# Kernel optimization log

Measured on AMD Instinct MI355X. Metric: run time of the kernel, lower is better.

## Reference

```python
import jax, jax.numpy as jnp
import numpy as np

N_GRAPHS = 128
N_NODES = 512
N = N_GRAPHS * N_NODES      # 65536 total nodes
E = 524288                  # edges (avg degree 8)
F_IN = 4                    # num_features
EMB = 4                     # embedding_dim
HEADS = 4
GDIM = 16                   # GATConv_dim
D = GDIM * HEADS            # 64 = d_model
NHEAD = 2                   # heads // 2
FF = 64                     # ff_hid_dim
OUT = 64                    # output_dim
N_GAT_REST = 3              # gat_layers - 1


def setup_inputs() -> dict:
    key = jax.random.key(0)
    ks = iter(jax.random.split(key, 64))
    def nrm(shape, fan_in):
        return jax.random.normal(next(ks), shape, jnp.float32) / np.float32(np.sqrt(fan_in))
    inp = {}
    inp['x'] = jax.random.normal(next(ks), (N, F_IN), jnp.float32)
    inp['edge_index'] = jax.random.randint(next(ks), (2, E), 0, N, dtype=jnp.int32)
    inp['batch'] = jnp.repeat(jnp.arange(N_GRAPHS, dtype=jnp.int32), N_NODES)
    # feature_fc
    inp['Wf'] = nrm((F_IN, EMB), F_IN); inp['bf'] = jnp.zeros((EMB,), jnp.float32)
    # input GATConv (EMB -> HEADS*GDIM)
    inp['gW0'] = nrm((EMB, HEADS * GDIM), EMB)
    inp['aS0'] = nrm((HEADS, GDIM), GDIM); inp['aD0'] = nrm((HEADS, GDIM), GDIM)
    inp['gb0'] = jnp.zeros((D,), jnp.float32)
    # remaining 3 GATConv layers (D -> HEADS*GDIM), stacked
    inp['gW'] = nrm((N_GAT_REST, D, HEADS * GDIM), D)
    inp['aS'] = nrm((N_GAT_REST, HEADS, GDIM), GDIM); inp['aD'] = nrm((N_GAT_REST, HEADS, GDIM), GDIM)
    inp['gb'] = jnp.zeros((N_GAT_REST, D), jnp.float32)
    # decoder layer: self-attn, cross-attn, layernorms, FFN
    for p in ['sWq','sWk','sWv','sWo','cWq','cWk','cWv','cWo']:
        inp[p] = nrm((D, D), D)
    for p in ['sbq','sbk','sbv','sbo','cbq','cbk','cbv','cbo']:
        inp[p] = jnp.zeros((D,), jnp.float32)
    for g, b in [('ln1g','ln1b'), ('ln2g','ln2b'), ('ln3g','ln3b')]:
        inp[g] = jnp.ones((D,), jnp.float32); inp[b] = jnp.zeros((D,), jnp.float32)
    inp['ffW1'] = nrm((D, FF), D); inp['ffb1'] = jnp.zeros((FF,), jnp.float32)
    inp['ffW2'] = nrm((FF, D), FF); inp['ffb2'] = jnp.zeros((D,), jnp.float32)
    inp['fcW'] = nrm((D, OUT), D); inp['fcb'] = jnp.zeros((OUT,), jnp.float32)
    return inp


def _gat(h_in, src, dst, W, a_s, a_d, b):
    # PyG GATConv, concat=True, negative_slope=0.2, self-loops already in (src,dst)
    h = (h_in @ W).reshape(N, HEADS, GDIM)
    es = jnp.einsum('nho,ho->nh', h, a_s)   # [N,H]
    ed = jnp.einsum('nho,ho->nh', h, a_d)
    e = jax.nn.leaky_relu(es[src] + ed[dst], 0.2)          # [E',H]
    m = jax.ops.segment_max(e, dst, num_segments=N)        # segment softmax over dst
    w = jnp.exp(e - m[dst])
    s = jax.ops.segment_sum(w, dst, num_segments=N)
    alpha = w / (s[dst] + 1e-16)
    out = jax.ops.segment_sum(h[src] * alpha[..., None], dst, num_segments=N)
    return out.reshape(N, D) + b


def _mha(q, kv, Wq, bq, Wk, bk, Wv, bv, Wo, bo):
    B, S, Dm = q.shape
    hd = Dm // NHEAD
    Q = (q @ Wq + bq).reshape(B, S, NHEAD, hd)
    K = (kv @ Wk + bk).reshape(B, S, NHEAD, hd)
    V = (kv @ Wv + bv).reshape(B, S, NHEAD, hd)
    a = jax.nn.softmax(jnp.einsum('bqhd,bkhd->bhqk', Q, K) / jnp.sqrt(jnp.float32(hd)), axis=-1)
    o = jnp.einsum('bhqk,bkhd->bqhd', a, V).reshape(B, S, Dm)
    return o @ Wo + bo


def _ln(x, g, b):
    m = x.mean(-1, keepdims=True)
    v = ((x - m) ** 2).mean(-1, keepdims=True)
    return (x - m) / jnp.sqrt(v + 1e-5) * g + b


def reference(x, edge_index, batch, Wf, bf, gW0, aS0, aD0, gb0, gW, aS, aD, gb,
              sWq, sWk, sWv, sWo, cWq, cWk, cWv, cWo,
              sbq, sbk, sbv, sbo, cbq, cbk, cbv, cbo,
              ln1g, ln1b, ln2g, ln2b, ln3g, ln3b,
              ffW1, ffb1, ffW2, ffb2, fcW, fcb):
    loops = jnp.arange(N, dtype=edge_index.dtype)
    src = jnp.concatenate([edge_index[0], loops])
    dst = jnp.concatenate([edge_index[1], loops])
    h = x @ Wf + bf
    h = jax.nn.leaky_relu(_gat(h, src, dst, gW0, aS0, aD0, gb0), 0.01)
    for i in range(N_GAT_REST):
        h = jax.nn.leaky_relu(_gat(h, src, dst, gW[i], aS[i], aD[i], gb[i]), 0.01)
    t = h.reshape(N_GRAPHS, N_NODES, D)
    # one transformer decoder layer, post-norm, memory = layer input
    mem = t
    t = _ln(t + _mha(t, t, sWq, sbq, sWk, sbk, sWv, sbv, sWo, sbo), ln1g, ln1b)
    t = _ln(t + _mha(t, mem, cWq, cbq, cWk, cbk, cWv, cbv, cWo, cbo), ln2g, ln2b)
    t = _ln(t + (jax.nn.relu(t @ ffW1 + ffb1) @ ffW2 + ffb2), ln3g, ln3b)
    h = t.reshape(N, D)
    pooled = jax.ops.segment_sum(h, batch, num_segments=N_GRAPHS) / jnp.float32(N_NODES)
    return pooled @ fcW + fcb
```

## Files before the change

### kernel.cpp

```cpp
#include <hip/hip_runtime.h>
#include <math.h>

#define NG 128
#define SEQ 512
#define NN 65536
#define EE 524288
#define DM 64

typedef __attribute__((ext_vector_type(8))) short short8;
typedef __attribute__((ext_vector_type(4))) float f32x4;

__device__ __forceinline__ float lrelu(float x, float s){ return x > 0.f ? x : s*x; }

__device__ __forceinline__ unsigned short f2bf(float x){
  union { float f; unsigned u; } v; v.f = x;
  unsigned r = v.u + 0x7FFF + ((v.u>>16)&1);
  return (unsigned short)(r>>16);
}
__device__ __forceinline__ float bf2f(unsigned short x){
  union { unsigned u; float f; } v; v.u = ((unsigned)x)<<16;
  return v.f;
}

__global__ void k_count(const int* __restrict__ dst, int* __restrict__ deg){
  int e = blockIdx.x*256 + threadIdx.x;
  atomicAdd(&deg[dst[e]], 1);
}

__global__ void k_scan1(const int* __restrict__ deg, int* __restrict__ excl, int* __restrict__ bsums){
  __shared__ int sm[256];
  int tid = threadIdx.x;
  int i = blockIdx.x*256 + tid;
  int v = deg[i];
  sm[tid] = v;
  __syncthreads();
  int val = v;
  for (int off=1; off<256; off<<=1){
    int add = (tid>=off)? sm[tid-off] : 0;
    __syncthreads();
    val += add;
    sm[tid] = val;
    __syncthreads();
  }
  excl[i] = val - v;
  if (tid==255) bsums[blockIdx.x] = val;
}

__global__ void k_scan2(int* __restrict__ bsums){
  __shared__ int sm[256];
  int tid=threadIdx.x;
  int v = bsums[tid];
  sm[tid]=v;
  __syncthreads();
  int val=v;
  for (int off=1; off<256; off<<=1){
    int add = (tid>=off)? sm[tid-off]:0;
    __syncthreads();
    val += add;
    sm[tid]=val;
    __syncthreads();
  }
  bsums[tid] = val - v;
}

__global__ void k_scan3(const int* __restrict__ excl, const int* __restrict__ bsums,
                        int* __restrict__ rowp, int* __restrict__ cursor){
  int i = blockIdx.x*256 + threadIdx.x;
  int v = excl[i] + bsums[blockIdx.x];
  rowp[i]=v; cursor[i]=v;
  if (i==0) rowp[NN]=EE;
}

__global__ void k_fill(const int* __restrict__ src, const int* __restrict__ dst,
                       int* __restrict__ cursor, int* __restrict__ col){
  int e = blockIdx.x*256 + threadIdx.x;
  int d = dst[e];
  int p = atomicAdd(&cursor[d], 1);
  col[p] = src[e];
}

__global__ void k_w0(const float* __restrict__ Wf, const float* __restrict__ bf,
                     const float* __restrict__ gW0, float* __restrict__ W0c, float* __restrict__ b0c){
  int j = threadIdx.x;
  float b = 0.f;
  for (int k=0;k<4;k++) b += bf[k]*gW0[k*64+j];
  b0c[j]=b;
  for (int i=0;i<4;i++){
    float s=0.f;
    for(int k=0;k<4;k++) s += Wf[i*4+k]*gW0[k*64+j];
    W0c[i*64+j]=s;
  }
}

template<int DIN, int BIAS>
__global__ void __launch_bounds__(256) k_transform(const float* __restrict__ hin, const float* __restrict__ W,
                            const float* __restrict__ bias,
                            const float* __restrict__ aSp, const float* __restrict__ aDp,
                            unsigned short* __restrict__ hout, float* __restrict__ es, float* __restrict__ ed){
  __shared__ float inL[DIN][68];
  __shared__ float Wl[DIN][64];
  __shared__ float asl[64], adl[64];
  int tid = threadIdx.x;
  int n0 = blockIdx.x*64;
  if (tid < 64){ asl[tid] = aSp[tid]; adl[tid] = aDp[tid]; }
  for (int idx=tid; idx<DIN*16; idx+=256){
    int k = idx>>4, jj = (idx&15)<<2;
    *(float4*)&Wl[k][jj] = *(const float4*)&W[k*64+jj];
  }
  for (int idx=tid; idx<64*(DIN/4); idx+=256){
    int node = idx/(DIN/4), kk = (idx%(DIN/4))*4;
    float4 v = *(const float4*)&hin[(size_t)(n0+node)*DIN + kk];
    inL[kk][node]=v.x; inL[kk+1][node]=v.y; inL[kk+2][node]=v.z; inL[kk+3][node]=v.w;
  }
  __syncthreads();
  int i = tid>>4, j = tid&15;
  float acc[4][4];
  #pragma unroll
  for (int r=0;r<4;r++){
    #pragma unroll
    for (int c=0;c<4;c++) acc[r][c] = 0.f;
  }
  #pragma unroll 4
  for (int k=0;k<DIN;k++){
    float4 av = *(float4*)&inL[k][4*i];
    float4 bv = *(float4*)&Wl[k][4*j];
    float a_[4]={av.x,av.y,av.z,av.w}, b_[4]={bv.x,bv.y,bv.z,bv.w};
    #pragma unroll
    for (int r=0;r<4;r++){
      #pragma unroll
      for (int c=0;c<4;c++) acc[r][c] += a_[r]*b_[c];
    }
  }
  float4 asv = *(float4*)&asl[4*j];
  float4 adv = *(float4*)&adl[4*j];
  float bb[4] = {0.f,0.f,0.f,0.f};
  if (BIAS){
    float4 bv = *(const float4*)&bias[4*j];
    bb[0]=bv.x; bb[1]=bv.y; bb[2]=bv.z; bb[3]=bv.w;
  }
  #pragma unroll
  for (int r=0;r<4;r++){
    float y0=acc[r][0]+bb[0], y1=acc[r][1]+bb[1], y2=acc[r][2]+bb[2], y3=acc[r][3]+bb[3];
    int node = n0 + 4*i + r;
    ushort4 hv;
    hv.x=f2bf(y0); hv.y=f2bf(y1); hv.z=f2bf(y2); hv.w=f2bf(y3);
    *(ushort4*)&hout[(size_t)node*64 + 4*j] = hv;
    float ps = y0*asv.x + y1*asv.y + y2*asv.z + y3*asv.w;
    float pd = y0*adv.x + y1*adv.y + y2*adv.z + y3*adv.w;
    ps += __shfl_xor(ps,1); ps += __shfl_xor(ps,2);
    pd += __shfl_xor(pd,1); pd += __shfl_xor(pd,2);
    if ((j&3)==0){
      es[(size_t)node*4 + (j>>2)] = ps;
      ed[(size_t)node*4 + (j>>2)] = pd;
    }
  }
}

__global__ void __launch_bounds__(256) k_transform_bf(const unsigned short* __restrict__ hin, const float* __restrict__ W,
                            const float* __restrict__ aSp, const float* __restrict__ aDp,
                            unsigned short* __restrict__ hout, float* __restrict__ es, float* __restrict__ ed){
  __shared__ float inL[64][68];
  __shared__ float Wl[64][64];
  __shared__ float asl[64], adl[64];
  int tid = threadIdx.x;
  int n0 = blockIdx.x*64;
  if (tid < 64){ asl[tid] = aSp[tid]; adl[tid] = aDp[tid]; }
  for (int idx=tid; idx<1024; idx+=256){
    int k = idx>>4, jj = (idx&15)<<2;
    *(float4*)&Wl[k][jj] = *(const float4*)&W[k*64+jj];
  }
  for (int idx=tid; idx<1024; idx+=256){
    int node = idx>>4, kk = (idx&15)<<2;
    ushort4 v = *(const ushort4*)&hin[(size_t)(n0+node)*64 + kk];
    inL[kk][node]=bf2f(v.x); inL[kk+1][node]=bf2f(v.y); inL[kk+2][node]=bf2f(v.z); inL[kk+3][node]=bf2f(v.w);
  }
  __syncthreads();
  int i = tid>>4, j = tid&15;
  float acc[4][4];
  #pragma unroll
  for (int r=0;r<4;r++){
    #pragma unroll
    for (int c=0;c<4;c++) acc[r][c] = 0.f;
  }
  #pragma unroll 4
  for (int k=0;k<64;k++){
    float4 av = *(float4*)&inL[k][4*i];
    float4 bv = *(float4*)&Wl[k][4*j];
    float a_[4]={av.x,av.y,av.z,av.w}, b_[4]={bv.x,bv.y,bv.z,bv.w};
    #pragma unroll
    for (int r=0;r<4;r++){
      #pragma unroll
      for (int c=0;c<4;c++) acc[r][c] += a_[r]*b_[c];
    }
  }
  float4 asv = *(float4*)&asl[4*j];
  float4 adv = *(float4*)&adl[4*j];
  #pragma unroll
  for (int r=0;r<4;r++){
    float y0=acc[r][0], y1=acc[r][1], y2=acc[r][2], y3=acc[r][3];
    int node = n0 + 4*i + r;
    ushort4 hv;
    hv.x=f2bf(y0); hv.y=f2bf(y1); hv.z=f2bf(y2); hv.w=f2bf(y3);
    *(ushort4*)&hout[(size_t)node*64 + 4*j] = hv;
    float ps = y0*asv.x + y1*asv.y + y2*asv.z + y3*asv.w;
    float pd = y0*adv.x + y1*adv.y + y2*adv.z + y3*adv.w;
    ps += __shfl_xor(ps,1); ps += __shfl_xor(ps,2);
    pd += __shfl_xor(pd,1); pd += __shfl_xor(pd,2);
    if ((j&3)==0){
      es[(size_t)node*4 + (j>>2)] = ps;
      ed[(size_t)node*4 + (j>>2)] = pd;
    }
  }
}

template<int BF16OUT>
__global__ void __launch_bounds__(256) k_aggregate(const unsigned short* __restrict__ h, const float* __restrict__ es,
                            const float* __restrict__ ed, const int* __restrict__ rowp,
                            const int* __restrict__ col, const float* __restrict__ gb,
                            void* __restrict__ houtv){
  int tid = threadIdx.x;
  int n = blockIdx.x*4 + (tid>>6);
  int l = tid&63;
  int q = l>>4;
  int sl = l&15;
  int head = sl>>2;
  float edn = ed[(size_t)n*4 + head];
  float es_self = es[(size_t)n*4 + head];
  int beg = __builtin_amdgcn_readfirstlane(rowp[n]);
  int end = __builtin_amdgcn_readfirstlane(rowp[n+1]);
  float m = -1e30f, s = 0.f;
  float a0=0.f, a1=0.f, a2=0.f, a3=0.f;
  int i = beg;
  for (; i+8 <= end; i += 8){
    int c0=col[i], c1=col[i+1], c2=col[i+2], c3=col[i+3];
    int c4=col[i+4], c5=col[i+5], c6=col[i+6], c7=col[i+7];
    int t01 = (q&1)? c1 : c0;
    int t23 = (q&1)? c3 : c2;
    int sq0 = (q&2)? t23 : t01;
    int t45 = (q&1)? c5 : c4;
    int t67 = (q&1)? c7 : c6;
    int sq1 = (q&2)? t67 : t45;
    ushort4 hv0 = *(const ushort4*)&h[(size_t)sq0*64 + 4*sl];
    ushort4 hv1 = *(const ushort4*)&h[(size_t)sq1*64 + 4*sl];
    float e0 = lrelu(es[(size_t)sq0*4+head] + edn, 0.2f);
    float e1 = lrelu(es[(size_t)sq1*4+head] + edn, 0.2f);
    float mx = fmaxf(e0, e1);
    if (__any(mx > m + 8.f)){
      float nm = fmaxf(m, mx);
      float c = __expf(m - nm);
      s*=c; a0*=c; a1*=c; a2*=c; a3*=c; m = nm;
    }
    float w0 = __expf(e0 - m);
    float w1 = __expf(e1 - m);
    s += w0 + w1;
    a0 += w0*bf2f(hv0.x) + w1*bf2f(hv1.x);
    a1 += w0*bf2f(hv0.y) + w1*bf2f(hv1.y);
    a2 += w0*bf2f(hv0.z) + w1*bf2f(hv1.z);
    a3 += w0*bf2f(hv0.w) + w1*bf2f(hv1.w);
  }
  if (i < end){
    int last = end-1;
    int i1=(i+1<last)?i+1:last, i2=(i+2<last)?i+2:last, i3=(i+3<last)?i+3:last;
    int i4=(i+4<last)?i+4:last, i5=(i+5<last)?i+5:last, i6=(i+6<last)?i+6:last;
    int c0=col[i], c1=col[i1], c2=col[i2], c3=col[i3];
    int c4=col[i4], c5=col[i5], c6=col[i6], c7=col[last];
    int t01 = (q&1)? c1 : c0;
    int t23 = (q&1)? c3 : c2;
    int sq0 = (q&2)? t23 : t01;
    int t45 = (q&1)? c5 : c4;
    int t67 = (q&1)? c7 : c6;
    int sq1 = (q&2)? t67 : t45;
    bool ac0 = (i + q) < end;
    bool ac1 = (i + 4 + q) < end;
    ushort4 hv0 = *(const ushort4*)&h[(size_t)sq0*64 + 4*sl];
    ushort4 hv1 = *(const ushort4*)&h[(size_t)sq1*64 + 4*sl];
    float e0 = lrelu(es[(size_t)sq0*4+head] + edn, 0.2f);
    float e1 = lrelu(es[(size_t)sq1*4+head] + edn, 0.2f);
    if (!ac0) e0 = -1e30f;
    if (!ac1) e1 = -1e30f;
    float mx = fmaxf(e0, e1);
    if (__any(mx > m + 8.f)){
      float nm = fmaxf(m, mx);
      float c = __expf(m - nm);
      s*=c; a0*=c; a1*=c; a2*=c; a3*=c; m = nm;
    }
    float w0 = ac0 ? __expf(e0 - m) : 0.f;
    float w1 = ac1 ? __expf(e1 - m) : 0.f;
    s += w0 + w1;
    a0 += w0*bf2f(hv0.x) + w1*bf2f(hv1.x);
    a1 += w0*bf2f(hv0.y) + w1*bf2f(hv1.y);
    a2 += w0*bf2f(hv0.z) + w1*bf2f(hv1.z);
    a3 += w0*bf2f(hv0.w) + w1*bf2f(hv1.w);
  }
  #pragma unroll
  for (int off=16; off<=32; off<<=1){
    float m2 = __shfl_xor(m, off);
    float s2 = __shfl_xor(s, off);
    float b0 = __shfl_xor(a0, off);
    float b1 = __shfl_xor(a1, off);
    float b2 = __shfl_xor(a2, off);
    float b3 = __shfl_xor(a3, off);
    float nm = fmaxf(m, m2);
    float c1 = __expf(m - nm), c2 = __expf(m2 - nm);
    s  = s*c1  + s2*c2;
    a0 = a0*c1 + b0*c2;
    a1 = a1*c1 + b1*c2;
    a2 = a2*c1 + b2*c2;
    a3 = a3*c1 + b3*c2;
    m = nm;
  }
  {
    float e_self = lrelu(es_self + edn, 0.2f);
    float nm = fmaxf(m, e_self);
    float c = __expf(m - nm), cs = __expf(e_self - nm);
    ushort4 hs = *(const ushort4*)&h[(size_t)n*64 + 4*sl];
    s  = s*c  + cs;
    a0 = a0*c + cs*bf2f(hs.x);
    a1 = a1*c + cs*bf2f(hs.y);
    a2 = a2*c + cs*bf2f(hs.z);
    a3 = a3*c + cs*bf2f(hs.w);
  }
  if (q == 0){
    float inv = 1.f/(s + 1e-16f);
    float4 gv = *(const float4*)&gb[4*sl];
    float o0 = lrelu(a0*inv + gv.x, 0.01f);
    float o1 = lrelu(a1*inv + gv.y, 0.01f);
    float o2 = lrelu(a2*inv + gv.z, 0.01f);
    float o3 = lrelu(a3*inv + gv.w, 0.01f);
    if (BF16OUT){
      ushort4 hv; hv.x=f2bf(o0); hv.y=f2bf(o1); hv.z=f2bf(o2); hv.w=f2bf(o3);
      *(ushort4*)((unsigned short*)houtv + (size_t)n*64 + 4*sl) = hv;
    } else {
      *(float4*)((float*)houtv + (size_t)n*64 + 4*sl) = make_float4(o0,o1,o2,o3);
    }
  }
}

__global__ void __launch_bounds__(256) k_qkv3(const float* __restrict__ in0, const float* __restrict__ W0, const float* __restrict__ b0, unsigned short* __restrict__ o0,
                      const float* __restrict__ in1, const float* __restrict__ W1, const float* __restrict__ b1, unsigned short* __restrict__ o1,
                      const float* __restrict__ in2, const float* __restrict__ W2, const float* __restrict__ b2, unsigned short* __restrict__ o2,
                      float scl0){
  __shared__ float inL[64][68];
  __shared__ float Wl[64][64];
  int tid = threadIdx.x;
  int n0 = blockIdx.x*64;
  int i = tid>>4, j = tid&15;
  const float* ins[3] = {in0, in1, in2};
  const float* Ws[3] = {W0, W1, W2};
  const float* bs[3] = {b0, b1, b2};
  unsigned short* os[3] = {o0, o1, o2};
  const float* cur = nullptr;
  for (int w=0; w<3; w++){
    __syncthreads();
    if (ins[w] != cur){
      cur = ins[w];
      for (int idx=tid; idx<1024; idx+=256){
        int node = idx>>4, kk = (idx&15)<<2;
        float4 v = *(const float4*)&cur[(size_t)(n0+node)*64 + kk];
        inL[kk][node]=v.x; inL[kk+1][node]=v.y; inL[kk+2][node]=v.z; inL[kk+3][node]=v.w;
      }
    }
    for (int idx=tid; idx<1024; idx+=256){
      int k = idx>>4, jj = (idx&15)<<2;
      *(float4*)&Wl[k][jj] = *(const float4*)&Ws[w][k*64+jj];
    }
    __syncthreads();
    float acc[4][4];
    #pragma unroll
    for (int r=0;r<4;r++){
      #pragma unroll
      for (int c=0;c<4;c++) acc[r][c] = 0.f;
    }
    #pragma unroll 4
    for (int k=0;k<64;k++){
      float4 av = *(float4*)&inL[k][4*i];
      float4 bv = *(float4*)&Wl[k][4*j];
      float a_[4]={av.x,av.y,av.z,av.w}, b_[4]={bv.x,bv.y,bv.z,bv.w};
      #pragma unroll
      for (int r=0;r<4;r++){
        #pragma unroll
        for (int c=0;c<4;c++) acc[r][c] += a_[r]*b_[c];
      }
    }
    float4 bv = *(const float4*)&bs[w][4*j];
    float bb[4] = {bv.x, bv.y, bv.z, bv.w};
    float sc = (w==0) ? scl0 : 1.f;
    #pragma unroll
    for (int r=0;r<4;r++){
      ushort4 hv;
      hv.x = f2bf((acc[r][0]+bb[0])*sc);
      hv.y = f2bf((acc[r][1]+bb[1])*sc);
      hv.z = f2bf((acc[r][2]+bb[2])*sc);
      hv.w = f2bf((acc[r][3]+bb[3])*sc);
      *(ushort4*)&os[w][(size_t)(n0+4*i+r)*64 + 4*j] = hv;
    }
  }
}

__global__ void __launch_bounds__(256) k_resln_bf(const unsigned short* __restrict__ in, const float* __restrict__ W,
                               const float* __restrict__ b, const float* __restrict__ res,
                               const float* __restrict__ g, const float* __restrict__ bl,
                               float* __restrict__ out){
  __shared__ float inL[64][68];
  __shared__ float Wl[64][64];
  int tid = threadIdx.x;
  int n0 = blockIdx.x*64;
  for (int idx=tid; idx<1024; idx+=256){
    int k = idx>>4, jj = (idx&15)<<2;
    *(float4*)&Wl[k][jj] = *(const float4*)&W[k*64+jj];
  }
  for (int idx=tid; idx<1024; idx+=256){
    int node = idx>>4, kk = (idx&15)<<2;
    ushort4 v = *(const ushort4*)&in[(size_t)(n0+node)*64 + kk];
    inL[kk][node]=bf2f(v.x); inL[kk+1][node]=bf2f(v.y); inL[kk+2][node]=bf2f(v.z); inL[kk+3][node]=bf2f(v.w);
  }
  __syncthreads();
  int i = tid>>4, j = tid&15;
  float acc[4][4];
  #pragma unroll
  for (int r=0;r<4;r++){
    #pragma unroll
    for (int c=0;c<4;c++) acc[r][c] = 0.f;
  }
  #pragma unroll 4
  for (int k=0;k<64;k++){
    float4 av = *(float4*)&inL[k][4*i];
    float4 bv = *(float4*)&Wl[k][4*j];
    float a_[4]={av.x,av.y,av.z,av.w}, b_[4]={bv.x,bv.y,bv.z,bv.w};
    #pragma unroll
    for (int r=0;r<4;r++){
      #pragma unroll
      for (int c=0;c<4;c++) acc[r][c] += a_[r]*b_[c];
    }
  }
  float4 bv = *(const float4*)&b[4*j];
  float bb[4] = {bv.x, bv.y, bv.z, bv.w};
  float4 gv = *(const float4*)&g[4*j];
  float4 blv = *(const float4*)&bl[4*j];
  float gg[4] = {gv.x, gv.y, gv.z, gv.w};
  float bb2[4] = {blv.x, blv.y, blv.z, blv.w};
  #pragma unroll
  for (int r=0;r<4;r++){
    int node = n0 + 4*i + r;
    float4 rv = *(const float4*)&res[(size_t)node*64 + 4*j];
    float y[4] = {acc[r][0]+bb[0]+rv.x, acc[r][1]+bb[1]+rv.y,
                  acc[r][2]+bb[2]+rv.z, acc[r][3]+bb[3]+rv.w};
    float s = (y[0]+y[1]) + (y[2]+y[3]);
    s += __shfl_xor(s,1); s += __shfl_xor(s,2); s += __shfl_xor(s,4); s += __shfl_xor(s,8);
    float mean = s * (1.f/64.f);
    float d[4] = {y[0]-mean, y[1]-mean, y[2]-mean, y[3]-mean};
    float v = (d[0]*d[0]+d[1]*d[1]) + (d[2]*d[2]+d[3]*d[3]);
    v += __shfl_xor(v,1); v += __shfl_xor(v,2); v += __shfl_xor(v,4); v += __shfl_xor(v,8);
    float inv = rsqrtf(v*(1.f/64.f) + 1e-5f);
    *(float4*)&out[(size_t)node*64 + 4*j] =
      make_float4(d[0]*inv*gg[0]+bb2[0], d[1]*inv*gg[1]+bb2[1],
                  d[2]*inv*gg[2]+bb2[2], d[3]*inv*gg[3]+bb2[3]);
  }
}

__global__ void __launch_bounds__(256) k_ffn(const float* __restrict__ in,
                     const float* __restrict__ W1p, const float* __restrict__ b1p,
                     const float* __restrict__ W2p, const float* __restrict__ b2p,
                     const float* __restrict__ g, const float* __restrict__ bl,
                     float* __restrict__ out){
  __shared__ float inL[64][68];
  __shared__ float Wl[64][64];
  __shared__ float ffL[64][68];
  int tid = threadIdx.x;
  int n0 = blockIdx.x*64;
  for (int idx=tid; idx<1024; idx+=256){
    int k = idx>>4, jj = (idx&15)<<2;
    *(float4*)&Wl[k][jj] = *(const float4*)&W1p[k*64+jj];
  }
  for (int idx=tid; idx<1024; idx+=256){
    int node = idx>>4, kk = (idx&15)<<2;
    float4 v = *(const float4*)&in[(size_t)(n0+node)*64 + kk];
    inL[kk][node]=v.x; inL[kk+1][node]=v.y; inL[kk+2][node]=v.z; inL[kk+3][node]=v.w;
  }
  __syncthreads();
  int i = tid>>4, j = tid&15;
  float acc[4][4];
  #pragma unroll
  for (int r=0;r<4;r++){
    #pragma unroll
    for (int c=0;c<4;c++) acc[r][c] = 0.f;
  }
  #pragma unroll 4
  for (int k=0;k<64;k++){
    float4 av = *(float4*)&inL[k][4*i];
    float4 bv = *(float4*)&Wl[k][4*j];
    float a_[4]={av.x,av.y,av.z,av.w}, b_[4]={bv.x,bv.y,bv.z,bv.w};
    #pragma unroll
    for (int r=0;r<4;r++){
      #pragma unroll
      for (int c=0;c<4;c++) acc[r][c] += a_[r]*b_[c];
    }
  }
  float4 b1v = *(const float4*)&b1p[4*j];
  float bb1[4] = {b1v.x, b1v.y, b1v.z, b1v.w};
  #pragma unroll
  for (int r=0;r<4;r++){
    #pragma unroll
    for (int c=0;c<4;c++){
      ffL[4*j+c][4*i+r] = fmaxf(acc[r][c] + bb1[c], 0.f);
    }
  }
  __syncthreads();
  for (int idx=tid; idx<1024; idx+=256){
    int k = idx>>4, jj = (idx&15)<<2;
    *(float4*)&Wl[k][jj] = *(const float4*)&W2p[k*64+jj];
  }
  __syncthreads();
  #pragma unroll
  for (int r=0;r<4;r++){
    #pragma unroll
    for (int c=0;c<4;c++) acc[r][c] = 0.f;
  }
  #pragma unroll 4
  for (int k=0;k<64;k++){
    float4 av = *(float4*)&ffL[k][4*i];
    float4 bv = *(float4*)&Wl[k][4*j];
    float a_[4]={av.x,av.y,av.z,av.w}, b_[4]={bv.x,bv.y,bv.z,bv.w};
    #pragma unroll
    for (int r=0;r<4;r++){
      #pragma unroll
      for (int c=0;c<4;c++) acc[r][c] += a_[r]*b_[c];
    }
  }
  float4 b2v = *(const float4*)&b2p[4*j];
  float bb2v[4] = {b2v.x, b2v.y, b2v.z, b2v.w};
  float4 gv = *(const float4*)&g[4*j];
  float4 blv = *(const float4*)&bl[4*j];
  float gg[4] = {gv.x, gv.y, gv.z, gv.w};
  float bbl[4] = {blv.x, blv.y, blv.z, blv.w};
  #pragma unroll
  for (int r=0;r<4;r++){
    int node = n0 + 4*i + r;
    float y[4];
    #pragma unroll
    for (int c=0;c<4;c++) y[c] = acc[r][c] + bb2v[c] + inL[4*j+c][4*i+r];
    float s = (y[0]+y[1]) + (y[2]+y[3]);
    s += __shfl_xor(s,1); s += __shfl_xor(s,2); s += __shfl_xor(s,4); s += __shfl_xor(s,8);
    float mean = s * (1.f/64.f);
    float d[4] = {y[0]-mean, y[1]-mean, y[2]-mean, y[3]-mean};
    float v = (d[0]*d[0]+d[1]*d[1]) + (d[2]*d[2]+d[3]*d[3]);
    v += __shfl_xor(v,1); v += __shfl_xor(v,2); v += __shfl_xor(v,4); v += __shfl_xor(v,8);
    float inv = rsqrtf(v*(1.f/64.f) + 1e-5f);
    *(float4*)&out[(size_t)node*64 + 4*j] =
      make_float4(d[0]*inv*gg[0]+bbl[0], d[1]*inv*gg[1]+bbl[1],
                  d[2]*inv*gg[2]+bbl[2], d[3]*inv*gg[3]+bbl[3]);
  }
}

__global__ void __launch_bounds__(512, 4) k_attn(const unsigned short* __restrict__ Q, const unsigned short* __restrict__ K,
                      const unsigned short* __restrict__ V, unsigned short* __restrict__ Out){
  __shared__ char smem[40960];
  char* Ksm = smem;
  char* Vsm = smem + 16384;
  char* Psm = smem + 32768;

  int bid = blockIdx.x;
  int qh = bid & 1;
  int h  = (bid>>1) & 1;
  int b  = bid>>2;
  int tid = threadIdx.x;
  int wave = tid>>6;
  int l = tid & 63;
  int lq = l & 15;
  int g  = l >> 4;
  const size_t hb = (size_t)b*SEQ*64 + (size_t)h*32;
  const f32x4 zero = {0.f,0.f,0.f,0.f};

  int qbase = qh*256 + wave*32;
  short8 qf[2];
  f32x4 O[2][2];
  float m_[2], l_[2];
  #pragma unroll
  for (int qt=0; qt<2; qt++){
    qf[qt] = *(const short8*)(Q + hb + (size_t)(qbase + qt*16 + lq)*64 + g*8);
    O[qt][0] = zero; O[qt][1] = zero;
    m_[qt] = -1e30f; l_[qt] = 0.f;
  }

  char* Pw = Psm + wave*1024;

  for (int ph=0; ph<2; ph++){
    __syncthreads();
    #pragma unroll
    for (int it=0; it<2; it++){
      int i = tid + it*512;
      int row = i>>2, j = i&3;
      uint4 v = *(const uint4*)(K + hb + (size_t)(ph*256 + row)*64 + j*8);
      *(uint4*)(Ksm + row*64 + ((j*16) ^ (((row>>1)&3)<<4))) = v;
    }
    #pragma unroll
    for (int it=0; it<2; it++){
      int i = tid + it*512;
      int key = i>>2, j = i&3;
      uint4 vv = *(const uint4*)(V + hb + (size_t)(ph*256 + key)*64 + j*8);
      const unsigned short* vs = (const unsigned short*)&vv;
      #pragma unroll
      for (int c=0;c<8;c++){
        int d = j*8 + c;
        *(unsigned short*)(Vsm + d*512 + ((key*2) ^ ((d&7)<<4))) = vs[c];
      }
    }
    __syncthreads();
    for (int p=0; p<8; p++){
      int r0 = p*32 + lq, r1 = r0 + 16;
      short8 kf0 = *(short8*)(Ksm + r0*64 + ((g*16) ^ (((r0>>1)&3)<<4)));
      short8 kf1 = *(short8*)(Ksm + r1*64 + ((g*16) ^ (((r1>>1)&3)<<4)));
      int d0 = lq, d1 = lq + 16;
      short8 vt0 = *(short8*)(Vsm + d0*512 + ((p*64 + g*16) ^ ((d0&7)<<4)));
      short8 vt1 = *(short8*)(Vsm + d1*512 + ((p*64 + g*16) ^ ((d1&7)<<4)));
      int swzp = ((lq>>1)&3)<<4;
      #pragma unroll
      for (int qt=0; qt<2; qt++){
        f32x4 s0 = __builtin_amdgcn_mfma_f32_16x16x32_bf16(kf0, qf[qt], zero, 0,0,0);
        f32x4 s1 = __builtin_amdgcn_mfma_f32_16x16x32_bf16(kf1, qf[qt], zero, 0,0,0);
        float pmax = fmaxf(fmaxf(fmaxf(s0.x,s0.y),fmaxf(s0.z,s0.w)),
                           fmaxf(fmaxf(s1.x,s1.y),fmaxf(s1.z,s1.w)));
        pmax = fmaxf(pmax, __shfl_xor(pmax, 16));
        pmax = fmaxf(pmax, __shfl_xor(pmax, 32));
        float mn = fmaxf(m_[qt], pmax);
        float corr = __expf(m_[qt] - mn);
        m_[qt] = mn;
        float e0 = __expf(s0.x - mn), e1 = __expf(s0.y - mn);
        float e2 = __expf(s0.z - mn), e3 = __expf(s0.w - mn);
        float e4 = __expf(s1.x - mn), e5 = __expf(s1.y - mn);
        float e6 = __expf(s1.z - mn), e7 = __expf(s1.w - mn);
        l_[qt] = l_[qt]*corr + (((e0+e1)+(e2+e3)) + ((e4+e5)+(e6+e7)));
        O[qt][0] *= corr; O[qt][1] *= corr;
        uint2 w0, w1;
        w0.x = (unsigned)f2bf(e0) | ((unsigned)f2bf(e1)<<16);
        w0.y = (unsigned)f2bf(e2) | ((unsigned)f2bf(e3)<<16);
        w1.x = (unsigned)f2bf(e4) | ((unsigned)f2bf(e5)<<16);
        w1.y = (unsigned)f2bf(e6) | ((unsigned)f2bf(e7)<<16);
        *(uint2*)(Pw + lq*64 + ((g*8) ^ swzp)) = w0;
        *(uint2*)(Pw + lq*64 + ((32 + g*8) ^ swzp)) = w1;
        short8 pb = *(short8*)(Pw + lq*64 + ((g*16) ^ swzp));
        O[qt][0] = __builtin_amdgcn_mfma_f32_16x16x32_bf16(vt0, pb, O[qt][0], 0,0,0);
        O[qt][1] = __builtin_amdgcn_mfma_f32_16x16x32_bf16(vt1, pb, O[qt][1], 0,0,0);
      }
    }
  }
  #pragma unroll
  for (int qt=0; qt<2; qt++){
    float lt = l_[qt];
    lt += __shfl_xor(lt, 16);
    lt += __shfl_xor(lt, 32);
    float inv = 1.f/lt;
    unsigned short* op = Out + hb + (size_t)(qbase + qt*16 + lq)*64;
    ushort4 o0, o1;
    o0.x=f2bf(O[qt][0].x*inv); o0.y=f2bf(O[qt][0].y*inv); o0.z=f2bf(O[qt][0].z*inv); o0.w=f2bf(O[qt][0].w*inv);
    o1.x=f2bf(O[qt][1].x*inv); o1.y=f2bf(O[qt][1].y*inv); o1.z=f2bf(O[qt][1].z*inv); o1.w=f2bf(O[qt][1].w*inv);
    *(ushort4*)(op + g*4) = o0;
    *(ushort4*)(op + 16 + g*4) = o1;
  }
}

__global__ void __launch_bounds__(256) k_pool_fc(const float* __restrict__ t, const float* __restrict__ fcW,
                          const float* __restrict__ fcb, float* __restrict__ out){
  __shared__ float pl[4][64];
  __shared__ float pf[64];
  int b = blockIdx.x;
  int tid = threadIdx.x;
  int j = tid&63, seg = tid>>6;
  const float* basep = t + (size_t)b*SEQ*64;
  float s = 0.f;
  for (int si=seg*128; si<(seg+1)*128; si++) s += basep[(size_t)si*64 + j];
  pl[seg][j] = s;
  __syncthreads();
  if (tid < 64){
    pf[tid] = (pl[0][tid]+pl[1][tid]+pl[2][tid]+pl[3][tid]) * (1.f/512.f);
  }
  __syncthreads();
  if (tid < 64){
    float o = fcb[tid];
    for (int k=0;k<64;k++) o += pf[k]*fcW[k*64+tid];
    out[(size_t)b*64 + tid] = o;
  }
}

extern "C" void kernel_launch(void* const* d_in, const int* in_sizes, int n_in,
                              void* d_out, int out_size, void* d_ws, size_t ws_size,
                              hipStream_t stream) {
  const float* x    = (const float*)d_in[0];
  const int*   ei   = (const int*)d_in[1];
  const float* Wf   = (const float*)d_in[3];
  const float* bf   = (const float*)d_in[4];
  const float* gW0  = (const float*)d_in[5];
  const float* aS0  = (const float*)d_in[6];
  const float* aD0  = (const float*)d_in[7];
  const float* gb0  = (const float*)d_in[8];
  const float* gW   = (const float*)d_in[9];
  const float* aS   = (const float*)d_in[10];
  const float* aD   = (const float*)d_in[11];
  const float* gb   = (const float*)d_in[12];
  const float* sWq  = (const float*)d_in[13];
  const float* sWk  = (const float*)d_in[14];
  const float* sWv  = (const float*)d_in[15];
  const float* sWo  = (const float*)d_in[16];
  const float* cWq  = (const float*)d_in[17];
  const float* cWk  = (const float*)d_in[18];
  const float* cWv  = (const float*)d_in[19];
  const float* cWo  = (const float*)d_in[20];
  const float* sbq  = (const float*)d_in[21];
  const float* sbk  = (const float*)d_in[22];
  const float* sbv  = (const float*)d_in[23];
  const float* sbo  = (const float*)d_in[24];
  const float* cbq  = (const float*)d_in[25];
  const float* cbk  = (const float*)d_in[26];
  const float* cbv  = (const float*)d_in[27];
  const float* cbo  = (const float*)d_in[28];
  const float* ln1g = (const float*)d_in[29];
  const float* ln1b = (const float*)d_in[30];
  const float* ln2g = (const float*)d_in[31];
  const float* ln2b = (const float*)d_in[32];
  const float* ln3g = (const float*)d_in[33];
  const float* ln3b = (const float*)d_in[34];
  const float* ffW1 = (const float*)d_in[35];
  const float* ffb1 = (const float*)d_in[36];
  const float* ffW2 = (const float*)d_in[37];
  const float* ffb2 = (const float*)d_in[38];
  const float* fcW  = (const float*)d_in[39];
  const float* fcb  = (const float*)d_in[40];

  char* ws = (char*)d_ws;
  size_t off = 0;
  auto alloc = [&](size_t bytes) -> void* {
    void* p = ws + off;
    off += (bytes + 255) & ~(size_t)255;
    return p;
  };
  int* deg    = (int*)alloc(NN*sizeof(int));
  int* excl   = (int*)alloc(NN*sizeof(int));
  int* rowp   = (int*)alloc((NN+1)*sizeof(int));
  int* cursor = (int*)alloc(NN*sizeof(int));
  int* col    = (int*)alloc(EE*sizeof(int));
  int* bsums  = (int*)alloc(256*sizeof(int));
  float* W0c  = (float*)alloc(4*64*sizeof(float));
  float* b0c  = (float*)alloc(64*sizeof(float));
  float* es   = (float*)alloc((size_t)NN*4*sizeof(float));
  float* ed   = (float*)alloc((size_t)NN*4*sizeof(float));
  unsigned short* Hb   = (unsigned short*)alloc((size_t)NN*64*sizeof(unsigned short));
  unsigned short* Hagg = (unsigned short*)alloc((size_t)NN*64*sizeof(unsigned short));
  unsigned short* Qb = (unsigned short*)alloc((size_t)NN*64*sizeof(unsigned short));
  unsigned short* Kb = (unsigned short*)alloc((size_t)NN*64*sizeof(unsigned short));
  unsigned short* Vb = (unsigned short*)alloc((size_t)NN*64*sizeof(unsigned short));
  unsigned short* Ob = (unsigned short*)alloc((size_t)NN*64*sizeof(unsigned short));
  float* B1   = (float*)alloc((size_t)NN*64*sizeof(float));
  float* B2   = (float*)alloc((size_t)NN*64*sizeof(float));
  float* B5   = (float*)alloc((size_t)NN*64*sizeof(float));

  const int* e_src = ei;
  const int* e_dst = ei + EE;

  const float scale = 0.17677669529663687f;

  hipMemsetAsync(deg, 0, NN*sizeof(int), stream);
  k_count<<<EE/256, 256, 0, stream>>>(e_dst, deg);
  k_scan1<<<NN/256, 256, 0, stream>>>(deg, excl, bsums);
  k_scan2<<<1, 256, 0, stream>>>(bsums);
  k_scan3<<<NN/256, 256, 0, stream>>>(excl, bsums, rowp, cursor);
  k_fill<<<EE/256, 256, 0, stream>>>(e_src, e_dst, cursor, col);

  k_w0<<<1, 64, 0, stream>>>(Wf, bf, gW0, W0c, b0c);

  k_transform<4,1><<<NN/64, 256, 0, stream>>>(x, W0c, b0c, aS0, aD0, Hb, es, ed);
  k_aggregate<1><<<NN/4, 256, 0, stream>>>(Hb, es, ed, rowp, col, gb0, Hagg);
  k_transform_bf<<<NN/64, 256, 0, stream>>>(Hagg, gW+0*4096, aS+0*64, aD+0*64, Hb, es, ed);
  k_aggregate<1><<<NN/4, 256, 0, stream>>>(Hb, es, ed, rowp, col, gb+0*64, Hagg);
  k_transform_bf<<<NN/64, 256, 0, stream>>>(Hagg, gW+1*4096, aS+1*64, aD+1*64, Hb, es, ed);
  k_aggregate<1><<<NN/4, 256, 0, stream>>>(Hb, es, ed, rowp, col, gb+1*64, Hagg);
  k_transform_bf<<<NN/64, 256, 0, stream>>>(Hagg, gW+2*4096, aS+2*64, aD+2*64, Hb, es, ed);
  k_aggregate<0><<<NN/4, 256, 0, stream>>>(Hb, es, ed, rowp, col, gb+2*64, B2);

  k_qkv3<<<NN/64, 256, 0, stream>>>(B2, sWq, sbq, Qb, B2, sWk, sbk, Kb, B2, sWv, sbv, Vb, scale);
  k_attn<<<NG*2*2, 512, 0, stream>>>(Qb, Kb, Vb, Ob);
  k_resln_bf<<<NN/64, 256, 0, stream>>>(Ob, sWo, sbo, B2, ln1g, ln1b, B5);

  k_qkv3<<<NN/64, 256, 0, stream>>>(B5, cWq, cbq, Qb, B2, cWk, cbk, Kb, B2, cWv, cbv, Vb, scale);
  k_attn<<<NG*2*2, 512, 0, stream>>>(Qb, Kb, Vb, Ob);
  k_resln_bf<<<NN/64, 256, 0, stream>>>(Ob, cWo, cbo, B5, ln2g, ln2b, B2);

  k_ffn<<<NN/64, 256, 0, stream>>>(B2, ffW1, ffb1, ffW2, ffb2, ln3g, ln3b, B1);

  k_pool_fc<<<NG, 256, 0, stream>>>(B1, fcW, fcb, (float*)d_out);
}
```

Baseline: 409.4 us.

## Interleave source attention scores into padded feature rows and fuse weight premultiply

The per-node source attention scores (es) are now stored inside each bf16 feature row, which is padded to a stride of 80 elements, instead of in a separate array. The aggregation gather can then fetch the neighbor's features and its score from the same row rather than making a second random access into another array. The tiny k_w0 launch is also folded into the first transform kernel, which recomputes the combined weight and bias per block. The cost is a 25% larger H buffer (160-byte rows) and some redundant per-block weight math.

```diff
diff --git a/kernel.cpp b/kernel.cpp
--- a/kernel.cpp
+++ b/kernel.cpp
@@ -6,6 +6,7 @@
 #define NN 65536
 #define EE 524288
 #define DM 64
+#define HSTR 80
 
 typedef __attribute__((ext_vector_type(8))) short short8;
 typedef __attribute__((ext_vector_type(4))) float f32x4;
@@ -79,38 +80,34 @@
   col[p] = src[e];
 }
 
-__global__ void k_w0(const float* __restrict__ Wf, const float* __restrict__ bf,
-                     const float* __restrict__ gW0, float* __restrict__ W0c, float* __restrict__ b0c){
-  int j = threadIdx.x;
-  float b = 0.f;
-  for (int k=0;k<4;k++) b += bf[k]*gW0[k*64+j];
-  b0c[j]=b;
-  for (int i=0;i<4;i++){
-    float s=0.f;
-    for(int k=0;k<4;k++) s += Wf[i*4+k]*gW0[k*64+j];
-    W0c[i*64+j]=s;
-  }
-}
-
-template<int DIN, int BIAS>
-__global__ void __launch_bounds__(256) k_transform(const float* __restrict__ hin, const float* __restrict__ W,
-                            const float* __restrict__ bias,
+__global__ void __launch_bounds__(256) k_transform0(const float* __restrict__ x,
+                            const float* __restrict__ Wf, const float* __restrict__ bf,
+                            const float* __restrict__ gW0,
                             const float* __restrict__ aSp, const float* __restrict__ aDp,
-                            unsigned short* __restrict__ hout, float* __restrict__ es, float* __restrict__ ed){
-  __shared__ float inL[DIN][68];
-  __shared__ float Wl[DIN][64];
+                            unsigned short* __restrict__ hout, float* __restrict__ ed){
+  __shared__ float inL[4][68];
+  __shared__ float Wl[4][64];
+  __shared__ float b0l[64];
   __shared__ float asl[64], adl[64];
   int tid = threadIdx.x;
   int n0 = blockIdx.x*64;
-  if (tid < 64){ asl[tid] = aSp[tid]; adl[tid] = aDp[tid]; }
-  for (int idx=tid; idx<DIN*16; idx+=256){
-    int k = idx>>4, jj = (idx&15)<<2;
-    *(float4*)&Wl[k][jj] = *(const float4*)&W[k*64+jj];
-  }
-  for (int idx=tid; idx<64*(DIN/4); idx+=256){
-    int node = idx/(DIN/4), kk = (idx%(DIN/4))*4;
-    float4 v = *(const float4*)&hin[(size_t)(n0+node)*DIN + kk];
-    inL[kk][node]=v.x; inL[kk+1][node]=v.y; inL[kk+2][node]=v.z; inL[kk+3][node]=v.w;
+  if (tid < 64){
+    asl[tid] = aSp[tid]; adl[tid] = aDp[tid];
+    float b = 0.f;
+    #pragma unroll
+    for (int k=0;k<4;k++) b += bf[k]*gW0[k*64+tid];
+    b0l[tid] = b;
+  }
+  {
+    int i = tid>>6, j = tid&63;
+    float s = 0.f;
+    #pragma unroll
+    for (int k=0;k<4;k++) s += Wf[i*4+k]*gW0[k*64+j];
+    Wl[i][j] = s;
+  }
+  if (tid < 64){
+    float4 v = *(const float4*)&x[(size_t)(n0+tid)*4];
+    inL[0][tid]=v.x; inL[1][tid]=v.y; inL[2][tid]=v.z; inL[3][tid]=v.w;
   }
   __syncthreads();
   int i = tid>>4, j = tid&15;
@@ -120,8 +117,8 @@
     #pragma unroll
     for (int c=0;c<4;c++) acc[r][c] = 0.f;
   }
-  #pragma unroll 4
-  for (int k=0;k<DIN;k++){
+  #pragma unroll
+  for (int k=0;k<4;k++){
     float4 av = *(float4*)&inL[k][4*i];
     float4 bv = *(float4*)&Wl[k][4*j];
     float a_[4]={av.x,av.y,av.z,av.w}, b_[4]={bv.x,bv.y,bv.z,bv.w};
@@ -133,24 +130,21 @@
   }
   float4 asv = *(float4*)&asl[4*j];
   float4 adv = *(float4*)&adl[4*j];
-  float bb[4] = {0.f,0.f,0.f,0.f};
-  if (BIAS){
-    float4 bv = *(const float4*)&bias[4*j];
-    bb[0]=bv.x; bb[1]=bv.y; bb[2]=bv.z; bb[3]=bv.w;
-  }
+  float4 bbv = *(float4*)&b0l[4*j];
+  float bb[4] = {bbv.x, bbv.y, bbv.z, bbv.w};
   #pragma unroll
   for (int r=0;r<4;r++){
     float y0=acc[r][0]+bb[0], y1=acc[r][1]+bb[1], y2=acc[r][2]+bb[2], y3=acc[r][3]+bb[3];
     int node = n0 + 4*i + r;
     ushort4 hv;
     hv.x=f2bf(y0); hv.y=f2bf(y1); hv.z=f2bf(y2); hv.w=f2bf(y3);
-    *(ushort4*)&hout[(size_t)node*64 + 4*j] = hv;
+    *(ushort4*)&hout[(size_t)node*HSTR + 4*j] = hv;
     float ps = y0*asv.x + y1*asv.y + y2*asv.z + y3*asv.w;
     float pd = y0*adv.x + y1*adv.y + y2*adv.z + y3*adv.w;
     ps += __shfl_xor(ps,1); ps += __shfl_xor(ps,2);
     pd += __shfl_xor(pd,1); pd += __shfl_xor(pd,2);
     if ((j&3)==0){
-      es[(size_t)node*4 + (j>>2)] = ps;
+      *(float*)&hout[(size_t)node*HSTR + 64 + 2*(j>>2)] = ps;
       ed[(size_t)node*4 + (j>>2)] = pd;
     }
   }
@@ -158,7 +152,7 @@
 
 __global__ void __launch_bounds__(256) k_transform_bf(const unsigned short* __restrict__ hin, const float* __restrict__ W,
                             const float* __restrict__ aSp, const float* __restrict__ aDp,
-                            unsigned short* __restrict__ hout, float* __restrict__ es, float* __restrict__ ed){
+                            unsigned short* __restrict__ hout, float* __restrict__ ed){
   __shared__ float inL[64][68];
   __shared__ float Wl[64][64];
   __shared__ float asl[64], adl[64];
@@ -201,20 +195,20 @@
     int node = n0 + 4*i + r;
     ushort4 hv;
     hv.x=f2bf(y0); hv.y=f2bf(y1); hv.z=f2bf(y2); hv.w=f2bf(y3);
-    *(ushort4*)&hout[(size_t)node*64 + 4*j] = hv;
+    *(ushort4*)&hout[(size_t)node*HSTR + 4*j] = hv;
     float ps = y0*asv.x + y1*asv.y + y2*asv.z + y3*asv.w;
     float pd = y0*adv.x + y1*adv.y + y2*adv.z + y3*adv.w;
     ps += __shfl_xor(ps,1); ps += __shfl_xor(ps,2);
     pd += __shfl_xor(pd,1); pd += __shfl_xor(pd,2);
     if ((j&3)==0){
-      es[(size_t)node*4 + (j>>2)] = ps;
+      *(float*)&hout[(size_t)node*HSTR + 64 + 2*(j>>2)] = ps;
       ed[(size_t)node*4 + (j>>2)] = pd;
     }
   }
 }
 
 template<int BF16OUT>
-__global__ void __launch_bounds__(256) k_aggregate(const unsigned short* __restrict__ h, const float* __restrict__ es,
+__global__ void __launch_bounds__(256) k_aggregate(const unsigned short* __restrict__ h,
                             const float* __restrict__ ed, const int* __restrict__ rowp,
                             const int* __restrict__ col, const float* __restrict__ gb,
                             void* __restrict__ houtv){
@@ -225,7 +219,7 @@
   int sl = l&15;
   int head = sl>>2;
   float edn = ed[(size_t)n*4 + head];
-  float es_self = es[(size_t)n*4 + head];
+  float es_self = *(const float*)&h[(size_t)n*HSTR + 64 + 2*head];
   int beg = __builtin_amdgcn_readfirstlane(rowp[n]);
   int end = __builtin_amdgcn_readfirstlane(rowp[n+1]);
   float m = -1e30f, s = 0.f;
@@ -240,10 +234,11 @@
     int t45 = (q&1)? c5 : c4;
     int t67 = (q&1)? c7 : c6;
     int sq1 = (q&2)? t67 : t45;
-    ushort4 hv0 = *(const ushort4*)&h[(size_t)sq0*64 + 4*sl];
-    ushort4 hv1 = *(const ushort4*)&h[(size_t)sq1*64 + 4*sl];
-    float e0 = lrelu(es[(size_t)sq0*4+head] + edn, 0.2f);
-    float e1 = lrelu(es[(size_t)sq1*4+head] + edn, 0.2f);
+    size_t b0r = (size_t)sq0*HSTR, b1r = (size_t)sq1*HSTR;
+    ushort4 hv0 = *(const ushort4*)&h[b0r + 4*sl];
+    ushort4 hv1 = *(const ushort4*)&h[b1r + 4*sl];
+    float e0 = lrelu(*(const float*)&h[b0r + 64 + 2*head] + edn, 0.2f);
+    float e1 = lrelu(*(const float*)&h[b1r + 64 + 2*head] + edn, 0.2f);
     float mx = fmaxf(e0, e1);
     if (__any(mx > m + 8.f)){
       float nm = fmaxf(m, mx);
@@ -272,10 +267,11 @@
     int sq1 = (q&2)? t67 : t45;
     bool ac0 = (i + q) < end;
     bool ac1 = (i + 4 + q) < end;
-    ushort4 hv0 = *(const ushort4*)&h[(size_t)sq0*64 + 4*sl];
-    ushort4 hv1 = *(const ushort4*)&h[(size_t)sq1*64 + 4*sl];
-    float e0 = lrelu(es[(size_t)sq0*4+head] + edn, 0.2f);
-    float e1 = lrelu(es[(size_t)sq1*4+head] + edn, 0.2f);
+    size_t b0r = (size_t)sq0*HSTR, b1r = (size_t)sq1*HSTR;
+    ushort4 hv0 = *(const ushort4*)&h[b0r + 4*sl];
+    ushort4 hv1 = *(const ushort4*)&h[b1r + 4*sl];
+    float e0 = lrelu(*(const float*)&h[b0r + 64 + 2*head] + edn, 0.2f);
+    float e1 = lrelu(*(const float*)&h[b1r + 64 + 2*head] + edn, 0.2f);
     if (!ac0) e0 = -1e30f;
     if (!ac1) e1 = -1e30f;
     float mx = fmaxf(e0, e1);
@@ -313,7 +309,7 @@
     float e_self = lrelu(es_self + edn, 0.2f);
     float nm = fmaxf(m, e_self);
     float c = __expf(m - nm), cs = __expf(e_self - nm);
-    ushort4 hs = *(const ushort4*)&h[(size_t)n*64 + 4*sl];
+    ushort4 hs = *(const ushort4*)&h[(size_t)n*HSTR + 4*sl];
     s  = s*c  + cs;
     a0 = a0*c + cs*bf2f(hs.x);
     a1 = a1*c + cs*bf2f(hs.y);
@@ -739,11 +735,8 @@
   int* cursor = (int*)alloc(NN*sizeof(int));
   int* col    = (int*)alloc(EE*sizeof(int));
   int* bsums  = (int*)alloc(256*sizeof(int));
-  float* W0c  = (float*)alloc(4*64*sizeof(float));
-  float* b0c  = (float*)alloc(64*sizeof(float));
-  float* es   = (float*)alloc((size_t)NN*4*sizeof(float));
   float* ed   = (float*)alloc((size_t)NN*4*sizeof(float));
-  unsigned short* Hb   = (unsigned short*)alloc((size_t)NN*64*sizeof(unsigned short));
+  unsigned short* Hb   = (unsigned short*)alloc((size_t)NN*HSTR*sizeof(unsigned short));
   unsigned short* Hagg = (unsigned short*)alloc((size_t)NN*64*sizeof(unsigned short));
   unsigned short* Qb = (unsigned short*)alloc((size_t)NN*64*sizeof(unsigned short));
   unsigned short* Kb = (unsigned short*)alloc((size_t)NN*64*sizeof(unsigned short));
@@ -765,16 +758,14 @@
   k_scan3<<<NN/256, 256, 0, stream>>>(excl, bsums, rowp, cursor);
   k_fill<<<EE/256, 256, 0, stream>>>(e_src, e_dst, cursor, col);
 
-  k_w0<<<1, 64, 0, stream>>>(Wf, bf, gW0, W0c, b0c);
-
-  k_transform<4,1><<<NN/64, 256, 0, stream>>>(x, W0c, b0c, aS0, aD0, Hb, es, ed);
-  k_aggregate<1><<<NN/4, 256, 0, stream>>>(Hb, es, ed, rowp, col, gb0, Hagg);
-  k_transform_bf<<<NN/64, 256, 0, stream>>>(Hagg, gW+0*4096, aS+0*64, aD+0*64, Hb, es, ed);
-  k_aggregate<1><<<NN/4, 256, 0, stream>>>(Hb, es, ed, rowp, col, gb+0*64, Hagg);
-  k_transform_bf<<<NN/64, 256, 0, stream>>>(Hagg, gW+1*4096, aS+1*64, aD+1*64, Hb, es, ed);
-  k_aggregate<1><<<NN/4, 256, 0, stream>>>(Hb, es, ed, rowp, col, gb+1*64, Hagg);
-  k_transform_bf<<<NN/64, 256, 0, stream>>>(Hagg, gW+2*4096, aS+2*64, aD+2*64, Hb, es, ed);
-  k_aggregate<0><<<NN/4, 256, 0, stream>>>(Hb, es, ed, rowp, col, gb+2*64, B2);
+  k_transform0<<<NN/64, 256, 0, stream>>>(x, Wf, bf, gW0, aS0, aD0, Hb, ed);
+  k_aggregate<1><<<NN/4, 256, 0, stream>>>(Hb, ed, rowp, col, gb0, Hagg);
+  k_transform_bf<<<NN/64, 256, 0, stream>>>(Hagg, gW+0*4096, aS+0*64, aD+0*64, Hb, ed);
+  k_aggregate<1><<<NN/4, 256, 0, stream>>>(Hb, ed, rowp, col, gb+0*64, Hagg);
+  k_transform_bf<<<NN/64, 256, 0, stream>>>(Hagg, gW+1*4096, aS+1*64, aD+1*64, Hb, ed);
+  k_aggregate<1><<<NN/4, 256, 0, stream>>>(Hb, ed, rowp, col, gb+1*64, Hagg);
+  k_transform_bf<<<NN/64, 256, 0, stream>>>(Hagg, gW+2*4096, aS+2*64, aD+2*64, Hb, ed);
+  k_aggregate<0><<<NN/4, 256, 0, stream>>>(Hb, ed, rowp, col, gb+2*64, B2);
 
   k_qkv3<<<NN/64, 256, 0, stream>>>(B2, sWq, sbq, Qb, B2, sWk, sbk, Kb, B2, sWv, sbv, Vb, scale);
   k_attn<<<NG*2*2, 512, 0, stream>>>(Qb, Kb, Vb, Ob);
```

New measurement: 412.1 us. About the same (+0.7%).
